# Optimization experiments

Hardware: AMD Instinct MI355X
Metric: run time of the kernel (lower is better)

## Reference

```python
import jax, jax.numpy as jnp
import numpy as np

N, H, W = 128, 192, 192
THING = 81            # cfg.MODEL.SOGNET.THING_NUM_CLASSES
CLS_DIM = 128         # cls_embedding_dim
POS_DIM = 64          # pos_embedding_dim
REL_DIM = CLS_DIM + POS_DIM


def setup_inputs() -> dict:
    key = jax.random.key(0)
    ks = jax.random.split(key, 8)
    mask_logits = jax.random.normal(ks[0], (1, N, H, W), dtype=jnp.float32)
    # valid boxes: x_max > x_min, y_max > y_min (log(w/h) must be finite)
    xy = jax.random.uniform(ks[1], (N, 2), minval=0.0, maxval=800.0)
    wh = jax.random.uniform(ks[2], (N, 2), minval=16.0, maxval=256.0)
    bbox = jnp.concatenate([xy, xy + wh], axis=1).astype(jnp.float32)
    cls_idx = jax.random.randint(ks[3], (N,), 1, THING)  # values in [1, 80]
    # params (kaiming-normal-ish scale)
    W_U = jax.random.normal(ks[4], (THING - 1, CLS_DIM), jnp.float32) * (2.0 / (THING - 1)) ** 0.5
    W_V = jax.random.normal(ks[5], (THING - 1, CLS_DIM), jnp.float32) * (2.0 / (THING - 1)) ** 0.5
    W_pos = jax.random.normal(ks[6], (4, POS_DIM), jnp.float32) * (2.0 / 4.0) ** 0.5
    W_P = jax.random.normal(ks[7], (REL_DIM, 1), jnp.float32) * (2.0 / REL_DIM) ** 0.5
    return {"mask_logits": mask_logits, "bbox": bbox, "W_U": W_U, "W_V": W_V,
            "W_pos": W_pos, "W_P": W_P, "cls_idx": cls_idx}


def _position_matrix(bbox):
    x_min, y_min, x_max, y_max = bbox[:, 0], bbox[:, 1], bbox[:, 2], bbox[:, 3]
    w = x_max - x_min
    h = y_max - y_min
    x_ctr = (x_min + x_max) / 2.0
    y_ctr = (y_min + y_max) / 2.0
    dx = -(x_ctr[:, None] - x_ctr[None, :]) / w[:, None]          # [N, N]
    dy = -(y_ctr[:, None] - y_ctr[None, :]) / h[:, None]
    dw = jnp.log(w[None, :] / w[:, None])                          # log(w_j / w_i)
    dh = jnp.log(h[None, :] / h[:, None])
    return jnp.stack([dx, dy, dw, dh], axis=2)                     # [N, N, 4]


def reference(mask_logits, bbox, W_U, W_V, W_pos, W_P, cls_idx):
    # --- class relation: outer product of two relu'd class embeddings ---
    one_hot = jax.nn.one_hot(cls_idx - 1, THING - 1, dtype=mask_logits.dtype)  # [N, 80]
    feat1 = jax.nn.relu(one_hot @ W_U)                             # [N, CLS_DIM]
    feat2 = jax.nn.relu(one_hot @ W_V)
    cls_rel = feat1[:, None, :] * feat2[None, :, :]                # [N, N, CLS_DIM]
    # --- position relation: 1x1 conv == linear over last dim ---
    pos_rel = jax.nn.relu(jnp.einsum('ijk,kd->ijd', _position_matrix(bbox), W_pos))  # [N, N, POS_DIM]
    # --- relation score ---
    relation_feat = jnp.concatenate([cls_rel, pos_rel], axis=2)    # [N, N, REL_DIM]
    overlap_score = jax.nn.sigmoid(jnp.einsum('ijk,k->ij', relation_feat, W_P[:, 0]))  # [N, N]
    relation_score = jax.nn.relu(overlap_score - overlap_score.T)  # [N, N]
    # --- relation-weighted mask aggregation ---
    # naive: sum_m (ml*mp)[b,n] * mp[b,m] * score[n,m]  -> factor the m-reduction as a GEMM
    mask_prob = jax.nn.sigmoid(mask_logits)                        # [1, N, H, W]
    weighted = jnp.einsum('nm,bmhw->bnhw', relation_score, mask_prob)
    overlap_part = mask_logits * mask_prob * weighted              # [1, N, H, W]
    return mask_logits - overlap_part
```

## Files before the change

kernel.cpp:

```cpp
#include <hip/hip_runtime.h>

#define N_OBJ 128
#define HW    36864
#define PX    144

typedef unsigned short u16;
typedef unsigned int   u32;

__device__ __forceinline__ float bf2f(u32 u) {
    union { u32 i; float f; } c; c.i = u << 16; return c.f;
}
__device__ __forceinline__ u16 f2bf(float f) {
    union { float f; u32 i; } c; c.f = f;
    u32 r = (c.i + 0x7fffu + ((c.i >> 16) & 1u)) >> 16;
    return (u16)r;
}
__device__ __forceinline__ u32 pack2(float a, float b) {
    return (u32)f2bf(a) | ((u32)f2bf(b) << 16);
}
__device__ __forceinline__ float sigf(float x) { return 1.0f / (1.0f + __expf(-x)); }

__device__ __forceinline__ void unpack8(uint4 v, float* o) {
    o[0] = bf2f(v.x & 0xffffu); o[1] = bf2f(v.x >> 16);
    o[2] = bf2f(v.y & 0xffffu); o[3] = bf2f(v.y >> 16);
    o[4] = bf2f(v.z & 0xffffu); o[5] = bf2f(v.z >> 16);
    o[6] = bf2f(v.w & 0xffffu); o[7] = bf2f(v.w >> 16);
}
__device__ __forceinline__ void unpack4(uint2 v, float* o) {
    o[0] = bf2f(v.x & 0xffffu); o[1] = bf2f(v.x >> 16);
    o[2] = bf2f(v.y & 0xffffu); o[3] = bf2f(v.y >> 16);
}

__device__ __forceinline__ float ldf(const void* p, int idx, int bf) {
    return bf ? bf2f((u32)((const u16*)p)[idx]) : ((const float*)p)[idx];
}

__global__ void k_detect(const u16* __restrict__ ml, u32* __restrict__ flag) {
    if (threadIdx.x == 0 && blockIdx.x == 0) {
        int sane = 0;
        for (int i = 0; i < 128; ++i) {
            u16 v = ml[i];
            u32 e = (v >> 7) & 0xffu;
            if ((v & 0x7fffu) == 0 || (e >= 90u && e <= 140u)) ++sane;
        }
        *flag = (sane >= 100) ? 1u : 0u;
    }
}

__global__ __launch_bounds__(128) void k_overlap(
    const void* __restrict__ bbox, const void* __restrict__ WU,
    const void* __restrict__ WV,   const void* __restrict__ Wpos,
    const void* __restrict__ WP,   const int* __restrict__ cls,
    const u32* __restrict__ flag,  float* __restrict__ ov)
{
    const int bf = (int)(*flag != 0);
    const int i = blockIdx.x, j = threadIdx.x;
    __shared__ float a_s[128];
    __shared__ float wpos_s[256];
    __shared__ float wpp_s[64];
    __shared__ float bbi_s[4];

    const int ci = cls[i] - 1;
    a_s[j] = fmaxf(ldf(WU, ci * 128 + j, bf), 0.f) * ldf(WP, j, bf);
    wpos_s[j]       = ldf(Wpos, j, bf);
    wpos_s[128 + j] = ldf(Wpos, 128 + j, bf);
    if (j < 64) wpp_s[j] = ldf(WP, 128 + j, bf);
    if (j < 4)  bbi_s[j] = ldf(bbox, i * 4 + j, bf);
    __syncthreads();

    const float xmi = bbi_s[0], ymi = bbi_s[1], xMi = bbi_s[2], yMi = bbi_s[3];
    const float wi = xMi - xmi, hi = yMi - ymi;
    const float xci = 0.5f * (xmi + xMi), yci = 0.5f * (ymi + yMi);

    const float xmj = ldf(bbox, j * 4 + 0, bf), ymj = ldf(bbox, j * 4 + 1, bf);
    const float xMj = ldf(bbox, j * 4 + 2, bf), yMj = ldf(bbox, j * 4 + 3, bf);
    const float wj = xMj - xmj, hj = yMj - ymj;
    const float xcj = 0.5f * (xmj + xMj), ycj = 0.5f * (ymj + yMj);

    const float p0 = -(xci - xcj) / wi;
    const float p1 = -(yci - ycj) / hi;
    const float p2 = __logf(wj / wi);
    const float p3 = __logf(hj / hi);

    float s = 0.f;
    const int cj = cls[j] - 1;
    #pragma unroll 8
    for (int c = 0; c < 128; ++c)
        s += a_s[c] * fmaxf(ldf(WV, cj * 128 + c, bf), 0.f);
    #pragma unroll 8
    for (int d = 0; d < 64; ++d) {
        float t = p0 * wpos_s[d] + p1 * wpos_s[64 + d] + p2 * wpos_s[128 + d] + p3 * wpos_s[192 + d];
        s += fmaxf(t, 0.f) * wpp_s[d];
    }
    ov[i * 128 + j] = sigf(s);
}

__global__ __launch_bounds__(128) void k_relT(
    const float* __restrict__ ov, u16* __restrict__ relT)
{
    const int m = blockIdx.x, n = threadIdx.x;
    float v = ov[n * 128 + m] - ov[m * 128 + n];
    relT[m * 128 + n] = f2bf(fmaxf(v, 0.f));
}

template<int BF16>
__global__ __launch_bounds__(256) void k_main(
    const void* __restrict__ mlv, const u16* __restrict__ relT,
    void* __restrict__ outv, const u32* __restrict__ flag)
{
    if ((*flag != 0) != (BF16 != 0)) return;

    __shared__ u16 rel_s[128 * 128];
    __shared__ u16 prob_s[64 * PX];

    const int tid = threadIdx.x;
    const int p0  = blockIdx.x * PX;

    {
        const uint4* src = (const uint4*)relT;
        uint4*       dst = (uint4*)rel_s;
        #pragma unroll
        for (int k = 0; k < 8; ++k) dst[tid + 256 * k] = src[tid + 256 * k];
    }

    const int g      = tid & 15;
    const int ng     = tid >> 4;
    const int n_base = ng * 8;
    const int pxA    = g * 4;
    const int pxB    = 64 + g * 4;
    const int pxC    = 128 + g;

    float acc[8][9];
    #pragma unroll
    for (int i = 0; i < 8; ++i)
        #pragma unroll
        for (int j = 0; j < 9; ++j) acc[i][j] = 0.f;

    for (int h = 0; h < 2; ++h) {
        if (h) __syncthreads();
        if (BF16) {
            const u16* ml = (const u16*)mlv;
            for (int idx = tid; idx < 64 * 18; idx += 256) {
                int r = idx / 18;
                int c = (idx % 18) * 8;
                int m = h * 64 + r;
                uint4 v = *(const uint4*)(ml + (size_t)m * HW + p0 + c);
                float f[8]; unpack8(v, f);
                uint4 o;
                o.x = pack2(sigf(f[0]), sigf(f[1]));
                o.y = pack2(sigf(f[2]), sigf(f[3]));
                o.z = pack2(sigf(f[4]), sigf(f[5]));
                o.w = pack2(sigf(f[6]), sigf(f[7]));
                *(uint4*)(prob_s + r * PX + c) = o;
            }
        } else {
            const float* ml = (const float*)mlv;
            for (int idx = tid; idx < 64 * 36; idx += 256) {
                int r = idx / 36;
                int c = (idx % 36) * 4;
                int m = h * 64 + r;
                float4 v = *(const float4*)(ml + (size_t)m * HW + p0 + c);
                uint2 o;
                o.x = pack2(sigf(v.x), sigf(v.y));
                o.y = pack2(sigf(v.z), sigf(v.w));
                *(uint2*)(prob_s + r * PX + c) = o;
            }
        }
        __syncthreads();

        for (int mm = 0; mm < 64; ++mm) {
            const int m = h * 64 + mm;
            uint4 ra  = *(const uint4*)(rel_s + m * 128 + n_base);
            uint2 rb0 = *(const uint2*)(prob_s + mm * PX + pxA);
            uint2 rb1 = *(const uint2*)(prob_s + mm * PX + pxB);
            u16   rb2 = prob_s[mm * PX + pxC];
            float a[8]; unpack8(ra, a);
            float b[9];
            unpack4(rb0, b); unpack4(rb1, b + 4);
            b[8] = bf2f((u32)rb2);
            #pragma unroll
            for (int i = 0; i < 8; ++i) {
                #pragma unroll
                for (int j = 0; j < 9; ++j)
                    acc[i][j] = fmaf(a[i], b[j], acc[i][j]);
            }
        }
    }

    #pragma unroll
    for (int i = 0; i < 8; ++i) {
        const int n = n_base + i;
        float mv[9];
        if (BF16) {
            const u16* mlr = (const u16*)mlv + (size_t)n * HW + p0;
            uint2 va = *(const uint2*)(mlr + pxA);
            uint2 vb = *(const uint2*)(mlr + pxB);
            unpack4(va, mv); unpack4(vb, mv + 4);
            mv[8] = bf2f((u32)mlr[pxC]);
        } else {
            const float* mlr = (const float*)mlv + (size_t)n * HW + p0;
            float4 va = *(const float4*)(mlr + pxA);
            float4 vb = *(const float4*)(mlr + pxB);
            mv[0] = va.x; mv[1] = va.y; mv[2] = va.z; mv[3] = va.w;
            mv[4] = vb.x; mv[5] = vb.y; mv[6] = vb.z; mv[7] = vb.w;
            mv[8] = mlr[pxC];
        }
        float o[9];
        #pragma unroll
        for (int j = 0; j < 9; ++j) {
            float pr = sigf(mv[j]);
            o[j] = mv[j] - mv[j] * pr * acc[i][j];
        }
        if (BF16) {
            u16* outr = (u16*)outv + (size_t)n * HW + p0;
            uint2 oa, ob;
            oa.x = pack2(o[0], o[1]); oa.y = pack2(o[2], o[3]);
            ob.x = pack2(o[4], o[5]); ob.y = pack2(o[6], o[7]);
            *(uint2*)(outr + pxA) = oa;
            *(uint2*)(outr + pxB) = ob;
            outr[pxC] = f2bf(o[8]);
        } else {
            float* outr = (float*)outv + (size_t)n * HW + p0;
            float4 oa, ob;
            oa.x = o[0]; oa.y = o[1]; oa.z = o[2]; oa.w = o[3];
            ob.x = o[4]; ob.y = o[5]; ob.z = o[6]; ob.w = o[7];
            *(float4*)(outr + pxA) = oa;
            *(float4*)(outr + pxB) = ob;
            outr[pxC] = o[8];
        }
    }
}

extern "C" void kernel_launch(void* const* d_in, const int* in_sizes, int n_in,
                              void* d_out, int out_size, void* d_ws, size_t ws_size,
                              hipStream_t stream) {
    const void* ml   = d_in[0];
    const void* bbox = d_in[1];
    const void* WU   = d_in[2];
    const void* WV   = d_in[3];
    const void* Wpos = d_in[4];
    const void* WP   = d_in[5];
    const int*  cls  = (const int*)d_in[6];

    u32*   flag = (u32*)d_ws;
    float* ov   = (float*)((char*)d_ws + 256);
    u16*   relT = (u16*)((char*)d_ws + 256 + 128 * 128 * 4);

    k_detect<<<dim3(1), dim3(64), 0, stream>>>((const u16*)ml, flag);
    k_overlap<<<dim3(128), dim3(128), 0, stream>>>(bbox, WU, WV, Wpos, WP, cls, flag, ov);
    k_relT<<<dim3(128), dim3(128), 0, stream>>>(ov, relT);
    k_main<1><<<dim3(256), dim3(256), 0, stream>>>(ml, relT, d_out, flag);
    k_main<0><<<dim3(256), dim3(256), 0, stream>>>(ml, relT, d_out, flag);
}
```

Before: 131.2 us.

## Use MFMA bf16 for relation-weighted GEMM and fuse relation-score kernels

Replaces the scalar FMA outer-product loop in the main kernel with MFMA 16x16x32 bf16 instructions, each wave owning a 32-row slice of objects across the 144-pixel tile. It also merges the overlap and transpose kernels into one that computes both directions of the score, and moves dtype detection into each kernel through a block-wide count, removing the separate detect kernel and its flag. The relation matrix in shared memory gets padded rows to cut bank conflicts. Costs: the B fragment is gathered with strided scalar shared-memory loads, and the epilogue now does uncoalesced scalar global loads and stores.

```diff
diff --git a/kernel.cpp b/kernel.cpp
--- a/kernel.cpp
+++ b/kernel.cpp
@@ -1,11 +1,13 @@
 #include <hip/hip_runtime.h>
 
-#define N_OBJ 128
 #define HW    36864
 #define PX    144
+#define RST   136
 
 typedef unsigned short u16;
 typedef unsigned int   u32;
+typedef __attribute__((ext_vector_type(8))) short bf16x8;
+typedef __attribute__((ext_vector_type(4))) float f32x4;
 
 __device__ __forceinline__ float bf2f(u32 u) {
     union { u32 i; float f; } c; c.i = u << 16; return c.f;
@@ -26,207 +28,173 @@
     o[4] = bf2f(v.z & 0xffffu); o[5] = bf2f(v.z >> 16);
     o[6] = bf2f(v.w & 0xffffu); o[7] = bf2f(v.w >> 16);
 }
-__device__ __forceinline__ void unpack4(uint2 v, float* o) {
-    o[0] = bf2f(v.x & 0xffffu); o[1] = bf2f(v.x >> 16);
-    o[2] = bf2f(v.y & 0xffffu); o[3] = bf2f(v.y >> 16);
-}
-
-__device__ __forceinline__ float ldf(const void* p, int idx, int bf) {
-    return bf ? bf2f((u32)((const u16*)p)[idx]) : ((const float*)p)[idx];
-}
-
-__global__ void k_detect(const u16* __restrict__ ml, u32* __restrict__ flag) {
-    if (threadIdx.x == 0 && blockIdx.x == 0) {
-        int sane = 0;
-        for (int i = 0; i < 128; ++i) {
-            u16 v = ml[i];
-            u32 e = (v >> 7) & 0xffu;
-            if ((v & 0x7fffu) == 0 || (e >= 90u && e <= 140u)) ++sane;
-        }
-        *flag = (sane >= 100) ? 1u : 0u;
-    }
-}
-
-__global__ __launch_bounds__(128) void k_overlap(
-    const void* __restrict__ bbox, const void* __restrict__ WU,
-    const void* __restrict__ WV,   const void* __restrict__ Wpos,
-    const void* __restrict__ WP,   const int* __restrict__ cls,
-    const u32* __restrict__ flag,  float* __restrict__ ov)
+
+template<int BF16>
+__device__ __forceinline__ float ld1(const void* p, int idx) {
+    return BF16 ? bf2f((u32)((const u16*)p)[idx]) : ((const float*)p)[idx];
+}
+
+template<int BF16>
+__device__ __forceinline__ bool wrong_dtype(const void* ml, int tid) {
+    int pred = 0;
+    if (tid < 128) {
+        u16 v = ((const u16*)ml)[tid];
+        u32 e = (v >> 7) & 0xffu;
+        pred = ((v & 0x7fffu) == 0 || (e >= 90u && e <= 140u)) ? 1 : 0;
+    }
+    int cnt = __syncthreads_count(pred);
+    return (cnt >= 100) != (BF16 != 0);
+}
+
+template<int BF16>
+__global__ __launch_bounds__(128) void k_rel(
+    const void* __restrict__ ml,   const void* __restrict__ bbox,
+    const void* __restrict__ WU,   const void* __restrict__ WV,
+    const void* __restrict__ Wpos, const void* __restrict__ WP,
+    const int* __restrict__ cls,   u16* __restrict__ relN)
 {
-    const int bf = (int)(*flag != 0);
-    const int i = blockIdx.x, j = threadIdx.x;
-    __shared__ float a_s[128];
-    __shared__ float wpos_s[256];
-    __shared__ float wpp_s[64];
-    __shared__ float bbi_s[4];
-
-    const int ci = cls[i] - 1;
-    a_s[j] = fmaxf(ldf(WU, ci * 128 + j, bf), 0.f) * ldf(WP, j, bf);
-    wpos_s[j]       = ldf(Wpos, j, bf);
-    wpos_s[128 + j] = ldf(Wpos, 128 + j, bf);
-    if (j < 64) wpp_s[j] = ldf(WP, 128 + j, bf);
-    if (j < 4)  bbi_s[j] = ldf(bbox, i * 4 + j, bf);
+    const int n = blockIdx.x, m = threadIdx.x;
+    if (wrong_dtype<BF16>(ml, m)) return;
+
+    __shared__ float u_s[128], v_s[128], wpos_s[256], wpp_s[64], bbn_s[4];
+
+    const int cn = cls[n] - 1;
+    {
+        float wp = ld1<BF16>(WP, m);
+        u_s[m] = fmaxf(ld1<BF16>(WU, cn * 128 + m), 0.f) * wp;
+        v_s[m] = fmaxf(ld1<BF16>(WV, cn * 128 + m), 0.f) * wp;
+    }
+    wpos_s[m]       = ld1<BF16>(Wpos, m);
+    wpos_s[128 + m] = ld1<BF16>(Wpos, 128 + m);
+    if (m < 64) wpp_s[m] = ld1<BF16>(WP, 128 + m);
+    if (m < 4)  bbn_s[m] = ld1<BF16>(bbox, n * 4 + m);
     __syncthreads();
 
-    const float xmi = bbi_s[0], ymi = bbi_s[1], xMi = bbi_s[2], yMi = bbi_s[3];
-    const float wi = xMi - xmi, hi = yMi - ymi;
-    const float xci = 0.5f * (xmi + xMi), yci = 0.5f * (ymi + yMi);
-
-    const float xmj = ldf(bbox, j * 4 + 0, bf), ymj = ldf(bbox, j * 4 + 1, bf);
-    const float xMj = ldf(bbox, j * 4 + 2, bf), yMj = ldf(bbox, j * 4 + 3, bf);
-    const float wj = xMj - xmj, hj = yMj - ymj;
-    const float xcj = 0.5f * (xmj + xMj), ycj = 0.5f * (ymj + yMj);
-
-    const float p0 = -(xci - xcj) / wi;
-    const float p1 = -(yci - ycj) / hi;
-    const float p2 = __logf(wj / wi);
-    const float p3 = __logf(hj / hi);
-
-    float s = 0.f;
-    const int cj = cls[j] - 1;
+    const int cm = cls[m] - 1;
+    float s1 = 0.f, s2 = 0.f;
     #pragma unroll 8
-    for (int c = 0; c < 128; ++c)
-        s += a_s[c] * fmaxf(ldf(WV, cj * 128 + c, bf), 0.f);
+    for (int c = 0; c < 128; ++c) {
+        float wv = ld1<BF16>(WV, cm * 128 + c);
+        float wu = ld1<BF16>(WU, cm * 128 + c);
+        s1 += u_s[c] * fmaxf(wv, 0.f);
+        s2 += v_s[c] * fmaxf(wu, 0.f);
+    }
+
+    const float xmn = bbn_s[0], ymn = bbn_s[1], xMn = bbn_s[2], yMn = bbn_s[3];
+    const float wn = xMn - xmn, hn = yMn - ymn;
+    const float xcn = 0.5f * (xmn + xMn), ycn = 0.5f * (ymn + yMn);
+    const float xmm = ld1<BF16>(bbox, m * 4 + 0), ymm = ld1<BF16>(bbox, m * 4 + 1);
+    const float xMm = ld1<BF16>(bbox, m * 4 + 2), yMm = ld1<BF16>(bbox, m * 4 + 3);
+    const float wm = xMm - xmm, hm = yMm - ymm;
+    const float xcm = 0.5f * (xmm + xMm), ycm = 0.5f * (ymm + yMm);
+
+    const float p0 = -(xcn - xcm) / wn, p1 = -(ycn - ycm) / hn;
+    const float p2 = __logf(wm / wn),   p3 = __logf(hm / hn);
+    const float q0 = -(xcm - xcn) / wm, q1 = -(ycm - ycn) / hm;
+    const float q2 = __logf(wn / wm),   q3 = __logf(hn / hm);
+
     #pragma unroll 8
     for (int d = 0; d < 64; ++d) {
-        float t = p0 * wpos_s[d] + p1 * wpos_s[64 + d] + p2 * wpos_s[128 + d] + p3 * wpos_s[192 + d];
-        s += fmaxf(t, 0.f) * wpp_s[d];
-    }
-    ov[i * 128 + j] = sigf(s);
-}
-
-__global__ __launch_bounds__(128) void k_relT(
-    const float* __restrict__ ov, u16* __restrict__ relT)
+        float w0 = wpos_s[d], w1 = wpos_s[64 + d], w2 = wpos_s[128 + d], w3 = wpos_s[192 + d];
+        float wp = wpp_s[d];
+        float t1 = p0 * w0 + p1 * w1 + p2 * w2 + p3 * w3;
+        float t2 = q0 * w0 + q1 * w1 + q2 * w2 + q3 * w3;
+        s1 += fmaxf(t1, 0.f) * wp;
+        s2 += fmaxf(t2, 0.f) * wp;
+    }
+
+    float r = fmaxf(sigf(s1) - sigf(s2), 0.f);
+    relN[n * 128 + m] = f2bf(r);
+}
+
+template<int BF16>
+__global__ __launch_bounds__(256) void k_main(
+    const void* __restrict__ mlv, const u16* __restrict__ relN,
+    void* __restrict__ outv)
 {
-    const int m = blockIdx.x, n = threadIdx.x;
-    float v = ov[n * 128 + m] - ov[m * 128 + n];
-    relT[m * 128 + n] = f2bf(fmaxf(v, 0.f));
-}
-
-template<int BF16>
-__global__ __launch_bounds__(256) void k_main(
-    const void* __restrict__ mlv, const u16* __restrict__ relT,
-    void* __restrict__ outv, const u32* __restrict__ flag)
-{
-    if ((*flag != 0) != (BF16 != 0)) return;
-
-    __shared__ u16 rel_s[128 * 128];
+    const int tid = threadIdx.x;
+    if (wrong_dtype<BF16>(mlv, tid)) return;
+
+    __shared__ u16 rel_s[128 * RST];
     __shared__ u16 prob_s[64 * PX];
 
-    const int tid = threadIdx.x;
-    const int p0  = blockIdx.x * PX;
-
-    {
-        const uint4* src = (const uint4*)relT;
-        uint4*       dst = (uint4*)rel_s;
+    const int px0 = blockIdx.x * PX;
+    const int w    = tid >> 6;
+    const int lane = tid & 63;
+    const int col  = lane & 15;
+    const int quad = lane >> 4;
+    const int n0   = w * 32;
+
+    for (int idx = tid; idx < 2048; idx += 256) {
+        int r = idx >> 4, c = idx & 15;
+        uint4 v = ((const uint4*)relN)[idx];
+        *(uint4*)(rel_s + r * RST + c * 8) = v;
+    }
+
+    f32x4 acc[2][9];
+    #pragma unroll
+    for (int i = 0; i < 2; ++i)
         #pragma unroll
-        for (int k = 0; k < 8; ++k) dst[tid + 256 * k] = src[tid + 256 * k];
-    }
-
-    const int g      = tid & 15;
-    const int ng     = tid >> 4;
-    const int n_base = ng * 8;
-    const int pxA    = g * 4;
-    const int pxB    = 64 + g * 4;
-    const int pxC    = 128 + g;
-
-    float acc[8][9];
-    #pragma unroll
-    for (int i = 0; i < 8; ++i)
+        for (int t = 0; t < 9; ++t) acc[i][t] = (f32x4){0.f, 0.f, 0.f, 0.f};
+
+    for (int h = 0; h < 2; ++h) {
+        __syncthreads();
+        for (int idx = tid; idx < 1152; idx += 256) {
+            int r = idx / 18, c = idx - r * 18;
+            size_t base = (size_t)(h * 64 + r) * HW + px0 + c * 8;
+            float f[8];
+            if (BF16) {
+                uint4 v = *(const uint4*)((const u16*)mlv + base);
+                unpack8(v, f);
+            } else {
+                float4 v0 = *(const float4*)((const float*)mlv + base);
+                float4 v1 = *(const float4*)((const float*)mlv + base + 4);
+                f[0] = v0.x; f[1] = v0.y; f[2] = v0.z; f[3] = v0.w;
+                f[4] = v1.x; f[5] = v1.y; f[6] = v1.z; f[7] = v1.w;
+            }
+            uint4 o;
+            o.x = pack2(sigf(f[0]), sigf(f[1]));
+            o.y = pack2(sigf(f[2]), sigf(f[3]));
+            o.z = pack2(sigf(f[4]), sigf(f[5]));
+            o.w = pack2(sigf(f[6]), sigf(f[7]));
+            *(uint4*)(prob_s + r * PX + c * 8) = o;
+        }
+        __syncthreads();
+
         #pragma unroll
-        for (int j = 0; j < 9; ++j) acc[i][j] = 0.f;
-
-    for (int h = 0; h < 2; ++h) {
-        if (h) __syncthreads();
-        if (BF16) {
-            const u16* ml = (const u16*)mlv;
-            for (int idx = tid; idx < 64 * 18; idx += 256) {
-                int r = idx / 18;
-                int c = (idx % 18) * 8;
-                int m = h * 64 + r;
-                uint4 v = *(const uint4*)(ml + (size_t)m * HW + p0 + c);
-                float f[8]; unpack8(v, f);
-                uint4 o;
-                o.x = pack2(sigf(f[0]), sigf(f[1]));
-                o.y = pack2(sigf(f[2]), sigf(f[3]));
-                o.z = pack2(sigf(f[4]), sigf(f[5]));
-                o.w = pack2(sigf(f[6]), sigf(f[7]));
-                *(uint4*)(prob_s + r * PX + c) = o;
-            }
-        } else {
-            const float* ml = (const float*)mlv;
-            for (int idx = tid; idx < 64 * 36; idx += 256) {
-                int r = idx / 36;
-                int c = (idx % 36) * 4;
-                int m = h * 64 + r;
-                float4 v = *(const float4*)(ml + (size_t)m * HW + p0 + c);
-                uint2 o;
-                o.x = pack2(sigf(v.x), sigf(v.y));
-                o.y = pack2(sigf(v.z), sigf(v.w));
-                *(uint2*)(prob_s + r * PX + c) = o;
+        for (int ksl = 0; ksl < 2; ++ksl) {
+            const int k0 = h * 64 + ksl * 32 + quad * 8;
+            bf16x8 a0 = *(const bf16x8*)(rel_s + (n0 + col) * RST + k0);
+            bf16x8 a1 = *(const bf16x8*)(rel_s + (n0 + 16 + col) * RST + k0);
+            const u16* bbase = prob_s + (ksl * 32 + quad * 8) * PX + col;
+            #pragma unroll
+            for (int t = 0; t < 9; ++t) {
+                const u16* bp = bbase + t * 16;
+                bf16x8 bfrag;
+                #pragma unroll
+                for (int j = 0; j < 8; ++j) bfrag[j] = (short)bp[j * PX];
+                acc[0][t] = __builtin_amdgcn_mfma_f32_16x16x32_bf16(a0, bfrag, acc[0][t], 0, 0, 0);
+                acc[1][t] = __builtin_amdgcn_mfma_f32_16x16x32_bf16(a1, bfrag, acc[1][t], 0, 0, 0);
             }
         }
-        __syncthreads();
-
-        for (int mm = 0; mm < 64; ++mm) {
-            const int m = h * 64 + mm;
-            uint4 ra  = *(const uint4*)(rel_s + m * 128 + n_base);
-            uint2 rb0 = *(const uint2*)(prob_s + mm * PX + pxA);
-            uint2 rb1 = *(const uint2*)(prob_s + mm * PX + pxB);
-            u16   rb2 = prob_s[mm * PX + pxC];
-            float a[8]; unpack8(ra, a);
-            float b[9];
-            unpack4(rb0, b); unpack4(rb1, b + 4);
-            b[8] = bf2f((u32)rb2);
+    }
+
+    #pragma unroll
+    for (int i = 0; i < 2; ++i) {
+        #pragma unroll
+        for (int t = 0; t < 9; ++t) {
+            const int nb = n0 + i * 16 + quad * 4;
+            const int px = px0 + t * 16 + col;
             #pragma unroll
-            for (int i = 0; i < 8; ++i) {
-                #pragma unroll
-                for (int j = 0; j < 9; ++j)
-                    acc[i][j] = fmaf(a[i], b[j], acc[i][j]);
+            for (int r = 0; r < 4; ++r) {
+                size_t off = (size_t)(nb + r) * HW + px;
+                float mlvv = BF16 ? bf2f((u32)((const u16*)mlv)[off])
+                                  : ((const float*)mlv)[off];
+                float pr = sigf(mlvv);
+                float o  = mlvv - mlvv * pr * acc[i][t][r];
+                if (BF16) ((u16*)outv)[off] = f2bf(o);
+                else      ((float*)outv)[off] = o;
             }
-        }
-    }
-
-    #pragma unroll
-    for (int i = 0; i < 8; ++i) {
-        const int n = n_base + i;
-        float mv[9];
-        if (BF16) {
-            const u16* mlr = (const u16*)mlv + (size_t)n * HW + p0;
-            uint2 va = *(const uint2*)(mlr + pxA);
-            uint2 vb = *(const uint2*)(mlr + pxB);
-            unpack4(va, mv); unpack4(vb, mv + 4);
-            mv[8] = bf2f((u32)mlr[pxC]);
-        } else {
-            const float* mlr = (const float*)mlv + (size_t)n * HW + p0;
-            float4 va = *(const float4*)(mlr + pxA);
-            float4 vb = *(const float4*)(mlr + pxB);
-            mv[0] = va.x; mv[1] = va.y; mv[2] = va.z; mv[3] = va.w;
-            mv[4] = vb.x; mv[5] = vb.y; mv[6] = vb.z; mv[7] = vb.w;
-            mv[8] = mlr[pxC];
-        }
-        float o[9];
-        #pragma unroll
-        for (int j = 0; j < 9; ++j) {
-            float pr = sigf(mv[j]);
-            o[j] = mv[j] - mv[j] * pr * acc[i][j];
-        }
-        if (BF16) {
-            u16* outr = (u16*)outv + (size_t)n * HW + p0;
-            uint2 oa, ob;
-            oa.x = pack2(o[0], o[1]); oa.y = pack2(o[2], o[3]);
-            ob.x = pack2(o[4], o[5]); ob.y = pack2(o[6], o[7]);
-            *(uint2*)(outr + pxA) = oa;
-            *(uint2*)(outr + pxB) = ob;
-            outr[pxC] = f2bf(o[8]);
-        } else {
-            float* outr = (float*)outv + (size_t)n * HW + p0;
-            float4 oa, ob;
-            oa.x = o[0]; oa.y = o[1]; oa.z = o[2]; oa.w = o[3];
-            ob.x = o[4]; ob.y = o[5]; ob.z = o[6]; ob.w = o[7];
-            *(float4*)(outr + pxA) = oa;
-            *(float4*)(outr + pxB) = ob;
-            outr[pxC] = o[8];
         }
     }
 }
@@ -242,13 +210,10 @@
     const void* WP   = d_in[5];
     const int*  cls  = (const int*)d_in[6];
 
-    u32*   flag = (u32*)d_ws;
-    float* ov   = (float*)((char*)d_ws + 256);
-    u16*   relT = (u16*)((char*)d_ws + 256 + 128 * 128 * 4);
-
-    k_detect<<<dim3(1), dim3(64), 0, stream>>>((const u16*)ml, flag);
-    k_overlap<<<dim3(128), dim3(128), 0, stream>>>(bbox, WU, WV, Wpos, WP, cls, flag, ov);
-    k_relT<<<dim3(128), dim3(128), 0, stream>>>(ov, relT);
-    k_main<1><<<dim3(256), dim3(256), 0, stream>>>(ml, relT, d_out, flag);
-    k_main<0><<<dim3(256), dim3(256), 0, stream>>>(ml, relT, d_out, flag);
-}
+    u16* relN = (u16*)d_ws;
+
+    k_rel<1><<<dim3(128), dim3(128), 0, stream>>>(ml, bbox, WU, WV, Wpos, WP, cls, relN);
+    k_rel<0><<<dim3(128), dim3(128), 0, stream>>>(ml, bbox, WU, WV, Wpos, WP, cls, relN);
+    k_main<1><<<dim3(256), dim3(256), 0, stream>>>(ml, relN, d_out);
+    k_main<0><<<dim3(256), dim3(256), 0, stream>>>(ml, relN, d_out);
+}
```

New measurement: 105.8 us (median of 2 runs). 19.3% less time.
